# Performance work log

Hardware: AMD Instinct MI355X
Metric: run time of the kernel (lower is better)

Reference implementation:

```python
import jax, jax.numpy as jnp
import numpy as np

NUM_CLASSES = 1000
B, Q, N = 64, 900, 30
NO_OBJ_W = 0.1
COST_CLASS, COST_BBOX, COST_GIOU = 1.0, 5.0, 2.0
LOSS_BBOX, LOSS_GIOU = 5.0, 2.0


def cxcywh_to_xyxy(b):
    cx, cy, w, h = b[..., 0], b[..., 1], b[..., 2], b[..., 3]
    return jnp.stack([cx - 0.5 * w, cy - 0.5 * h, cx + 0.5 * w, cy + 0.5 * h], axis=-1)


def _area(b):
    return jnp.clip(b[..., 2] - b[..., 0], 0.0) * jnp.clip(b[..., 3] - b[..., 1], 0.0)


def giou_xyxy(b1, b2):
    # GIoU over broadcastable [..., 4] xyxy boxes
    lt = jnp.maximum(b1[..., :2], b2[..., :2])
    rb = jnp.minimum(b1[..., 2:], b2[..., 2:])
    wh = jnp.clip(rb - lt, 0.0)
    inter = wh[..., 0] * wh[..., 1]
    union = _area(b1) + _area(b2) - inter
    iou = inter / jnp.maximum(union, 1e-6)
    ltc = jnp.minimum(b1[..., :2], b2[..., :2])
    rbc = jnp.maximum(b1[..., 2:], b2[..., 2:])
    whc = jnp.clip(rbc - ltc, 0.0)
    ac = whc[..., 0] * whc[..., 1]
    return iou - (ac - union) / jnp.maximum(ac, 1e-6)


def _cost_matrices(pred_logits, pred_boxes, tgt_labels, tgt_boxes_xyxy):
    prob = jax.nn.softmax(pred_logits, axis=-1)                    # [B,Q,C+1]
    cost_cls = -jax.vmap(lambda p, l: p[:, l])(prob, tgt_labels)   # [B,Q,N]
    pred_xyxy = jnp.clip(cxcywh_to_xyxy(pred_boxes), 0.0, 1.0)     # [B,Q,4]
    cost_l1 = jnp.sum(jnp.abs(pred_xyxy[:, :, None] - tgt_boxes_xyxy[:, None]), -1)
    cost_g = -giou_xyxy(pred_xyxy[:, :, None], tgt_boxes_xyxy[:, None])
    C = COST_CLASS * cost_cls + COST_BBOX * cost_l1 + COST_GIOU * cost_g
    return C, pred_xyxy


def greedy_match(C):
    # faithful to the module's torch fallback matcher: iteratively pick the
    # global minimum of the cost matrix, masking used rows/cols (host-side,
    # non-differentiable, exactly like the detach->cpu->assignment in torch)
    Cw = C.copy()
    Qn, Nn = Cw.shape
    rows, cols = [], []
    for _ in range(min(Qn, Nn)):
        i = int(np.argmin(Cw))
        pi, ti = divmod(i, Nn)
        rows.append(pi)
        cols.append(ti)
        Cw[pi, :] = 1e9
        Cw[:, ti] = 1e9
    return np.array(rows, dtype=np.int32), np.array(cols, dtype=np.int32)


def match_all(Cnp):
    pis, tis = zip(*[greedy_match(Cnp[b]) for b in range(Cnp.shape[0])])
    return jnp.asarray(np.stack(pis)), jnp.asarray(np.stack(tis))  # [B,N] each


def set_losses(pred_logits, pred_xyxy, tgt_labels, tgt_boxes_xyxy, pi, ti):
    ce_weight = jnp.ones(NUM_CLASSES + 1, jnp.float32).at[NUM_CLASSES].set(NO_OBJ_W)
    bidx = jnp.arange(B)[:, None]
    # target class per query: matched -> tgt label, else no-object class
    tc = jnp.full((B, Q), NUM_CLASSES, dtype=jnp.int32)
    tc = tc.at[bidx, pi].set(jnp.take_along_axis(tgt_labels, ti, axis=1))
    nll = -jnp.take_along_axis(jax.nn.log_softmax(pred_logits, -1), tc[..., None].astype(jnp.int32), axis=2)[..., 0]
    w = ce_weight[tc]
    ce = jnp.mean(jnp.sum(w * nll, axis=1) / jnp.sum(w, axis=1))  # torch weighted CE mean, per image
    p_m = pred_xyxy[bidx, pi]          # [B,N,4] matched preds
    t_m = tgt_boxes_xyxy[bidx, ti]     # [B,N,4] matched targets
    l1 = jnp.mean(jnp.mean(jnp.abs(p_m - t_m), axis=(1, 2)))
    gl = jnp.mean(jnp.mean(1.0 - giou_xyxy(p_m, t_m), axis=1))
    total = ce + LOSS_BBOX * l1 + LOSS_GIOU * gl
    return jnp.stack([total, ce, l1, gl])


def setup_inputs():
    key = jax.random.key(0)
    k1, k2, k3, k4, k5 = jax.random.split(key, 5)
    pred_logits = jax.random.normal(k1, (B, Q, NUM_CLASSES + 1), jnp.float32)
    pred_boxes = jax.random.uniform(k2, (B, Q, 4), jnp.float32, 0.05, 0.95)
    tgt_labels = jax.random.randint(k3, (B, N), 0, NUM_CLASSES, dtype=jnp.int32)
    lt = jax.random.uniform(k4, (B, N, 2), jnp.float32, 0.0, 0.6)
    wh = jax.random.uniform(k5, (B, N, 2), jnp.float32, 0.02, 0.37)
    tgt_boxes_xyxy = jnp.concatenate([lt, lt + wh], axis=-1)  # valid 0..1 xyxy
    return {"pred_logits": pred_logits, "pred_boxes": pred_boxes,
            "tgt_labels": tgt_labels, "tgt_boxes_xyxy": tgt_boxes_xyxy}


def reference(pred_logits, pred_boxes, tgt_labels, tgt_boxes_xyxy):
    C, pred_xyxy = _cost_matrices(pred_logits, pred_boxes, tgt_labels, tgt_boxes_xyxy)
    pi, ti = match_all(np.asarray(jax.lax.stop_gradient(C)))
    # returns [loss_total, loss_ce, loss_bbox, loss_giou]
    return set_losses(pred_logits, pred_xyxy, tgt_labels, tgt_boxes_xyxy, pi, ti)
```

## Files before the change

kernel.cpp:

```cpp
#include <hip/hip_runtime.h>
#include <math.h>

#define BB 64
#define QQ 900
#define NN 30
#define C1 1001
#define QN (QQ * NN)
#define NO_OBJ_W 0.1f

__device__ __align__(16) unsigned g_ordT[BB * NN * QQ];
__device__ unsigned long long g_top[BB * NN * NN];
__device__ float  g_logZ[BB * QQ];
__device__ float  g_noobj[BB * QQ];
__device__ float4 g_xyxy[BB * QQ];
__device__ float  g_acc[3];
__device__ unsigned g_cnt;

__device__ __forceinline__ float giou_f(float ax1, float ay1, float ax2, float ay2,
                                        float bx1, float by1, float bx2, float by2) {
    float ix1 = fmaxf(ax1, bx1), iy1 = fmaxf(ay1, by1);
    float ix2 = fminf(ax2, bx2), iy2 = fminf(ay2, by2);
    float iw = fmaxf(ix2 - ix1, 0.f), ih = fmaxf(iy2 - iy1, 0.f);
    float inter = iw * ih;
    float areaA = fmaxf(ax2 - ax1, 0.f) * fmaxf(ay2 - ay1, 0.f);
    float areaB = fmaxf(bx2 - bx1, 0.f) * fmaxf(by2 - by1, 0.f);
    float uni = areaA + areaB - inter;
    float iou = inter / fmaxf(uni, 1e-6f);
    float cx1 = fminf(ax1, bx1), cy1 = fminf(ay1, by1);
    float cx2 = fmaxf(ax2, bx2), cy2 = fmaxf(ay2, by2);
    float cw = fmaxf(cx2 - cx1, 0.f), ch = fmaxf(cy2 - cy1, 0.f);
    float ac = cw * ch;
    return iou - (ac - uni) / fmaxf(ac, 1e-6f);
}

__device__ __forceinline__ unsigned ord_map(float f) {
    unsigned u = __float_as_uint(f);
    return (u & 0x80000000u) ? ~u : (u | 0x80000000u);
}

__global__ __launch_bounds__(256) void cost_kernel(const float* __restrict__ logits,
                                                   const float* __restrict__ pboxes,
                                                   const int*   __restrict__ labels,
                                                   const float* __restrict__ tboxes) {
    if (blockIdx.x == 0 && threadIdx.x == 0) {
        g_acc[0] = 0.f; g_acc[1] = 0.f; g_acc[2] = 0.f;
        g_cnt = 0u;
    }
    int tid = threadIdx.x;
    int lane = tid & 63, wid = tid >> 6;
    int gwave = blockIdx.x * 4 + wid;
    int b = gwave / QQ;

    __shared__ unsigned s_c[4][NN];

    size_t s = (size_t)gwave * C1;
    size_t a0 = (s + 3) >> 2;
    size_t a1 = (s + C1) >> 2;
    int nq = (int)(a1 - a0);
    int hh = (int)(a0 * 4 - s);
    int tt = (int)((s + C1) - a1 * 4);

    int lab = 0;
    float rl = 0.f;
    if (lane < NN) {
        lab = labels[b * NN + lane];
        rl = logits[s + lab];
    }
    float row1000 = logits[s + 1000];
    float4 tbv = make_float4(0.f, 0.f, 0.f, 0.f);
    if (lane < NN) tbv = *(const float4*)(tboxes + ((size_t)(b * NN + lane)) * 4);

    const float4* L4 = (const float4*)logits;
    float4 v4[4];
#pragma unroll
    for (int i = 0; i < 4; ++i) {
        int qq = lane + 64 * i;
        v4[i] = (qq < nq) ? L4[a0 + qq]
                          : make_float4(-INFINITY, -INFINITY, -INFINITY, -INFINITY);
    }
    float e1 = (lane < hh) ? logits[s + lane] : -INFINITY;
    float e2 = (lane < tt) ? logits[a1 * 4 + lane] : -INFINITY;

    float sm = __expf(e1) + __expf(e2);
#pragma unroll
    for (int i = 0; i < 4; ++i) {
        sm += __expf(v4[i].x);
        sm += __expf(v4[i].y);
        sm += __expf(v4[i].z);
        sm += __expf(v4[i].w);
    }
#pragma unroll
    for (int off = 32; off; off >>= 1) sm += __shfl_xor(sm, off);
    float logZ = __logf(sm);

    const float* pb = pboxes + (size_t)gwave * 4;
    float cx = pb[0], cy = pb[1], w = pb[2], h = pb[3];
    float x1 = fminf(fmaxf(cx - 0.5f * w, 0.f), 1.f);
    float y1 = fminf(fmaxf(cy - 0.5f * h, 0.f), 1.f);
    float x2 = fminf(fmaxf(cx + 0.5f * w, 0.f), 1.f);
    float y2 = fminf(fmaxf(cy + 0.5f * h, 0.f), 1.f);

    if (lane == 0) {
        g_logZ[gwave] = logZ;
        g_noobj[gwave] = logZ - row1000;
        g_xyxy[gwave] = make_float4(x1, y1, x2, y2);
    }

    if (lane < NN) {
        int t = lane;
        float pcls = __expf(rl - logZ);
        float tx1 = tbv.x, ty1 = tbv.y, tx2 = tbv.z, ty2 = tbv.w;
        float l1 = fabsf(x1 - tx1) + fabsf(y1 - ty1) + fabsf(x2 - tx2) + fabsf(y2 - ty2);
        float g = giou_f(x1, y1, x2, y2, tx1, ty1, tx2, ty2);
        s_c[wid][t] = ord_map(-pcls + 5.0f * l1 - 2.0f * g);
    }
    __syncthreads();

    if (tid < NN) {
        int t = tid;
        int q0 = (blockIdx.x % 225) * 4;
        int b0 = blockIdx.x / 225;
        uint4 v = make_uint4(s_c[0][t], s_c[1][t], s_c[2][t], s_c[3][t]);
        *(uint4*)&g_ordT[((size_t)(b0 * NN + t)) * QQ + q0] = v;
    }
}

__global__ __launch_bounds__(256) void select_kernel() {
    int gw = (blockIdx.x * blockDim.x + threadIdx.x) >> 6;
    int lane = threadIdx.x & 63;
    if (gw >= BB * NN) return;
    int t = gw % NN;

    const unsigned* col = g_ordT + (size_t)gw * QQ;
    unsigned long long key[16];
#pragma unroll
    for (int j = 0; j < 15; ++j) {
        int q = j * 64 + lane;
        if (q < QQ) {
            unsigned o = col[q];
            key[j] = ((unsigned long long)o << 32) | (unsigned)(q * NN + t);
        } else {
            key[j] = ~0ull;
        }
    }
    key[15] = ~0ull;

#pragma unroll
    for (int kk = 2; kk <= 16; kk <<= 1) {
#pragma unroll
        for (int jj = kk >> 1; jj > 0; jj >>= 1) {
#pragma unroll
            for (int i = 0; i < 16; ++i) {
                int l = i ^ jj;
                if (l > i) {
                    bool up = ((i & kk) == 0);
                    unsigned long long a = key[i], c = key[l];
                    bool sw = up ? (a > c) : (a < c);
                    key[i] = sw ? c : a;
                    key[l] = sw ? a : c;
                }
            }
        }
    }

    unsigned long long* outp = g_top + (size_t)gw * NN;
#pragma unroll 1
    for (int r = 0; r < NN / 2; ++r) {
        unsigned long long m1 = key[0];
        unsigned long long m2 = key[1];
#pragma unroll
        for (int off = 32; off; off >>= 1) {
            unsigned long long o1 = __shfl_xor(m1, off);
            unsigned long long o2 = __shfl_xor(m2, off);
            unsigned long long lo = (o1 < m1) ? o1 : m1;
            unsigned long long hi = (o1 < m1) ? m1 : o1;
            unsigned long long n2 = (o2 < m2) ? o2 : m2;
            m1 = lo;
            m2 = (hi < n2) ? hi : n2;
        }
        if (lane == 2 * r)     outp[2 * r]     = m1;
        if (lane == 2 * r + 1) outp[2 * r + 1] = m2;
        if (key[0] == m1 || key[0] == m2) {
#pragma unroll
            for (int j = 0; j < 15; ++j) key[j] = key[j + 1];
            key[15] = ~0ull;
        }
        if (key[0] == m2) {
#pragma unroll
            for (int j = 0; j < 15; ++j) key[j] = key[j + 1];
            key[15] = ~0ull;
        }
    }
}

__global__ __launch_bounds__(256) void match_loss_kernel(const float* __restrict__ logits,
                                                         const int*   __restrict__ labels,
                                                         const float* __restrict__ tboxes,
                                                         float* __restrict__ out) {
    int b = blockIdx.x;
    int tid = threadIdx.x;

    __shared__ unsigned long long s_cand[NN * NN];
    __shared__ int s_pi[NN], s_ti[NN];
    __shared__ unsigned s_dead[29];
    __shared__ float s4[4][4];

    const unsigned long long* topb = g_top + (size_t)b * NN * NN;
    for (int i = tid; i < NN * NN; i += 256) s_cand[i] = topb[i];
    if (tid < 29) s_dead[tid] = 0u;
    __syncthreads();

    if (tid < 64) {
        int lane = tid;
        bool colLive = lane < NN;
        int ptr = 0;
        unsigned long long cand = colLive ? s_cand[lane * NN] : ~0ull;
        unsigned rowc = colLive ? ((unsigned)cand) / NN : 0u;

        int it = 0;
        while (it < NN) {
            unsigned long long m1 = colLive ? cand : ~0ull;
            unsigned long long m2 = ~0ull;
#pragma unroll
            for (int off = 32; off; off >>= 1) {
                unsigned long long o1 = __shfl_xor(m1, off);
                unsigned long long o2 = __shfl_xor(m2, off);
                unsigned long long lo = (o1 < m1) ? o1 : m1;
                unsigned long long hi = (o1 < m1) ? m1 : o1;
                unsigned long long n2 = (o2 < m2) ? o2 : m2;
                m1 = lo;
                m2 = (hi < n2) ? hi : n2;
            }
            unsigned e1 = (unsigned)m1;
            int q1 = e1 / NN, t1 = e1 - (e1 / NN) * NN;
            unsigned e2 = (unsigned)m2;
            int q2 = e2 / NN, t2 = e2 - (e2 / NN) * NN;
            bool acc2 = (m2 != ~0ull) && (it + 1 < NN) && (q2 != q1) && (t2 != t1);

            if (lane == 0) {
                s_pi[it] = q1;
                s_ti[it] = t1;
                s_dead[q1 >> 5] |= (1u << (q1 & 31));
                if (acc2) {
                    s_pi[it + 1] = q2;
                    s_ti[it + 1] = t2;
                    s_dead[q2 >> 5] |= (1u << (q2 & 31));
                }
            }
            if (lane == t1) colLive = false;
            if (acc2 && lane == t2) colLive = false;
            if (colLive && (rowc == (unsigned)q1 || (acc2 && rowc == (unsigned)q2))) {
                do {
                    ++ptr;
                    cand = s_cand[lane * NN + ptr];
                    rowc = ((unsigned)cand) / NN;
                } while ((s_dead[rowc >> 5] >> (rowc & 31)) & 1u);
            }
            it += acc2 ? 2 : 1;
        }
    }
    __syncthreads();

    float sA = 0.f;
    for (int q = tid; q < QQ; q += 256) sA += g_noobj[b * QQ + q];

    float sB = 0.f, sL = 0.f, sG = 0.f;
    if (tid < NN) {
        int pq = s_pi[tid], pt = s_ti[tid];
        int gq = b * QQ + pq;
        int lab = labels[b * NN + pt];
        float mnll = g_logZ[gq] - logits[(size_t)gq * C1 + lab];
        sB = mnll - NO_OBJ_W * g_noobj[gq];
        float4 p = g_xyxy[gq];
        const float* tb = tboxes + ((size_t)(b * NN + pt)) * 4;
        float tx1 = tb[0], ty1 = tb[1], tx2 = tb[2], ty2 = tb[3];
        sL = fabsf(p.x - tx1) + fabsf(p.y - ty1) + fabsf(p.z - tx2) + fabsf(p.w - ty2);
        sG = 1.0f - giou_f(p.x, p.y, p.z, p.w, tx1, ty1, tx2, ty2);
    }

    int lane = tid & 63, wid = tid >> 6;
    float vv[4] = {sA, sB, sL, sG};
#pragma unroll
    for (int j = 0; j < 4; ++j) {
        float x = vv[j];
#pragma unroll
        for (int off = 32; off; off >>= 1) x += __shfl_xor(x, off);
        if (lane == 0) s4[wid][j] = x;
    }
    __syncthreads();
    if (tid == 0) {
        float a = 0.f, bs = 0.f, l = 0.f, g = 0.f;
        for (int w = 0; w < 4; ++w) { a += s4[w][0]; bs += s4[w][1]; l += s4[w][2]; g += s4[w][3]; }
        atomicAdd(&g_acc[0], NO_OBJ_W * a + bs);
        atomicAdd(&g_acc[1], l);
        atomicAdd(&g_acc[2], g);
        __threadfence();
        unsigned prev = atomicAdd(&g_cnt, 1u);
        if (prev == BB - 1) {
            __threadfence();
            float ce = atomicAdd(&g_acc[0], 0.f) / (float)(BB * 117);
            float l1 = atomicAdd(&g_acc[1], 0.f) / (float)(BB * NN * 4);
            float gl = atomicAdd(&g_acc[2], 0.f) / (float)(BB * NN);
            out[0] = ce + 5.0f * l1 + 2.0f * gl;
            out[1] = ce;
            out[2] = l1;
            out[3] = gl;
        }
    }
}

extern "C" void kernel_launch(void* const* d_in, const int* in_sizes, int n_in,
                              void* d_out, int out_size, void* d_ws, size_t ws_size,
                              hipStream_t stream) {
    const float* pred_logits = (const float*)d_in[0];
    const float* pred_boxes  = (const float*)d_in[1];
    const int*   tgt_labels  = (const int*)d_in[2];
    const float* tgt_boxes   = (const float*)d_in[3];
    float* out = (float*)d_out;

    cost_kernel<<<(BB * QQ) / 4, 256, 0, stream>>>(pred_logits, pred_boxes, tgt_labels, tgt_boxes);
    select_kernel<<<(BB * NN) / 4, 256, 0, stream>>>();
    match_loss_kernel<<<BB, 256, 0, stream>>>(pred_logits, tgt_labels, tgt_boxes, out);
}
```

Before: 84.80 us.

## Split per-column top-k selection across two waves and merge halves

The select kernel now gives each cost column to two waves, each sorting and extracting the top 30 from half of the 900 queries. The two sorted halves are then merged by rank using binary search in shared memory. This halves the register sort depth and per-wave serial extraction at the cost of twice as many waves plus a merge step. The no-object sum in the match kernel is also moved onto the idle waves so it runs alongside the serial greedy matching.

```diff
diff --git a/kernel.cpp b/kernel.cpp
--- a/kernel.cpp
+++ b/kernel.cpp
@@ -7,6 +7,7 @@
 #define C1 1001
 #define QN (QQ * NN)
 #define NO_OBJ_W 0.1f
+#define HQ 450
 
 __device__ __align__(16) unsigned g_ordT[BB * NN * QQ];
 __device__ unsigned long long g_top[BB * NN * NN];
@@ -60,10 +61,9 @@
     int hh = (int)(a0 * 4 - s);
     int tt = (int)((s + C1) - a1 * 4);
 
-    int lab = 0;
     float rl = 0.f;
     if (lane < NN) {
-        lab = labels[b * NN + lane];
+        int lab = labels[b * NN + lane];
         rl = logits[s + lab];
     }
     float row1000 = logits[s + 1000];
@@ -107,12 +107,10 @@
     }
 
     if (lane < NN) {
-        int t = lane;
         float pcls = __expf(rl - logZ);
-        float tx1 = tbv.x, ty1 = tbv.y, tx2 = tbv.z, ty2 = tbv.w;
-        float l1 = fabsf(x1 - tx1) + fabsf(y1 - ty1) + fabsf(x2 - tx2) + fabsf(y2 - ty2);
-        float g = giou_f(x1, y1, x2, y2, tx1, ty1, tx2, ty2);
-        s_c[wid][t] = ord_map(-pcls + 5.0f * l1 - 2.0f * g);
+        float l1 = fabsf(x1 - tbv.x) + fabsf(y1 - tbv.y) + fabsf(x2 - tbv.z) + fabsf(y2 - tbv.w);
+        float g = giou_f(x1, y1, x2, y2, tbv.x, tbv.y, tbv.z, tbv.w);
+        s_c[wid][lane] = ord_map(-pcls + 5.0f * l1 - 2.0f * g);
     }
     __syncthreads();
 
@@ -126,31 +124,37 @@
 }
 
 __global__ __launch_bounds__(256) void select_kernel() {
-    int gw = (blockIdx.x * blockDim.x + threadIdx.x) >> 6;
-    int lane = threadIdx.x & 63;
-    if (gw >= BB * NN) return;
+    int tid = threadIdx.x;
+    int lane = tid & 63, wid = tid >> 6;
+    int gw = blockIdx.x * 2 + (wid >> 1);
+    int h = wid & 1;
     int t = gw % NN;
 
-    const unsigned* col = g_ordT + (size_t)gw * QQ;
-    unsigned long long key[16];
-#pragma unroll
-    for (int j = 0; j < 15; ++j) {
-        int q = j * 64 + lane;
-        if (q < QQ) {
-            unsigned o = col[q];
-            key[j] = ((unsigned long long)o << 32) | (unsigned)(q * NN + t);
-        } else {
-            key[j] = ~0ull;
-        }
-    }
-    key[15] = ~0ull;
-
-#pragma unroll
-    for (int kk = 2; kk <= 16; kk <<= 1) {
+    __shared__ unsigned long long s_half[4][NN];
+
+    const unsigned* col = g_ordT + (size_t)gw * QQ + h * HQ;
+    int qbase = h * HQ;
+
+    unsigned long long key[8];
+#pragma unroll
+    for (int j = 0; j < 7; ++j) {
+        int ql = j * 64 + lane;
+        unsigned o = col[ql];
+        key[j] = ((unsigned long long)o << 32) | (unsigned)((qbase + ql) * NN + t);
+    }
+    {
+        int ql = 448 + lane;
+        key[7] = (lane < 2)
+            ? (((unsigned long long)col[ql] << 32) | (unsigned)((qbase + ql) * NN + t))
+            : ~0ull;
+    }
+
+#pragma unroll
+    for (int kk = 2; kk <= 8; kk <<= 1) {
 #pragma unroll
         for (int jj = kk >> 1; jj > 0; jj >>= 1) {
 #pragma unroll
-            for (int i = 0; i < 16; ++i) {
+            for (int i = 0; i < 8; ++i) {
                 int l = i ^ jj;
                 if (l > i) {
                     bool up = ((i & kk) == 0);
@@ -163,7 +167,6 @@
         }
     }
 
-    unsigned long long* outp = g_top + (size_t)gw * NN;
 #pragma unroll 1
     for (int r = 0; r < NN / 2; ++r) {
         unsigned long long m1 = key[0];
@@ -178,17 +181,38 @@
             m1 = lo;
             m2 = (hi < n2) ? hi : n2;
         }
-        if (lane == 2 * r)     outp[2 * r]     = m1;
-        if (lane == 2 * r + 1) outp[2 * r + 1] = m2;
+        if (lane == 2 * r)     s_half[wid][2 * r]     = m1;
+        if (lane == 2 * r + 1) s_half[wid][2 * r + 1] = m2;
         if (key[0] == m1 || key[0] == m2) {
 #pragma unroll
-            for (int j = 0; j < 15; ++j) key[j] = key[j + 1];
-            key[15] = ~0ull;
+            for (int j = 0; j < 7; ++j) key[j] = key[j + 1];
+            key[7] = ~0ull;
         }
         if (key[0] == m2) {
 #pragma unroll
-            for (int j = 0; j < 15; ++j) key[j] = key[j + 1];
-            key[15] = ~0ull;
+            for (int j = 0; j < 7; ++j) key[j] = key[j + 1];
+            key[7] = ~0ull;
+        }
+    }
+    __syncthreads();
+
+    if ((wid & 1) == 0) {
+        const unsigned long long* A = s_half[wid];
+        const unsigned long long* B = s_half[wid + 1];
+        unsigned long long mykey = ~0ull;
+        const unsigned long long* other = B;
+        int myidx = -1;
+        if (lane < NN)                  { mykey = A[lane];      other = B; myidx = lane; }
+        else if (lane >= 32 && lane < 32 + NN) { mykey = B[lane - 32]; other = A; myidx = lane - 32; }
+        if (myidx >= 0) {
+            int lo = 0, hi = NN;
+            while (lo < hi) {
+                int mid = (lo + hi) >> 1;
+                if (other[mid] < mykey) lo = mid + 1;
+                else hi = mid;
+            }
+            int pos = myidx + lo;
+            if (pos < NN) g_top[(size_t)gw * NN + pos] = mykey;
         }
     }
 }
@@ -210,7 +234,10 @@
     if (tid < 29) s_dead[tid] = 0u;
     __syncthreads();
 
-    if (tid < 64) {
+    float sA = 0.f;
+    if (tid >= 64) {
+        for (int q = tid - 64; q < QQ; q += 192) sA += g_noobj[b * QQ + q];
+    } else {
         int lane = tid;
         bool colLive = lane < NN;
         int ptr = 0;
@@ -260,9 +287,6 @@
         }
     }
     __syncthreads();
-
-    float sA = 0.f;
-    for (int q = tid; q < QQ; q += 256) sA += g_noobj[b * QQ + q];
 
     float sB = 0.f, sL = 0.f, sG = 0.f;
     if (tid < NN) {
@@ -319,6 +343,6 @@
     float* out = (float*)d_out;
 
     cost_kernel<<<(BB * QQ) / 4, 256, 0, stream>>>(pred_logits, pred_boxes, tgt_labels, tgt_boxes);
-    select_kernel<<<(BB * NN) / 4, 256, 0, stream>>>();
+    select_kernel<<<(BB * NN) / 2, 256, 0, stream>>>();
     match_loss_kernel<<<BB, 256, 0, stream>>>(pred_logits, tgt_labels, tgt_boxes, out);
 }
```

Result: slower. 92.75 us (+9.4%).

## Replace per-column bitonic top-k with histogram threshold selection plus small sort

Applied to the files above, without the earlier changes.

The select kernel now finds the 30 smallest costs per target column differently. It builds a 256-bin shared-memory histogram over the column's value range, finds the bin holding the 30th element with a prefix scan, compacts the candidates at or below that bin with ballot, and bitonic-sorts up to 64 of them across the wave. If more than 64 candidates fall at or below the threshold, it falls back to the old register sort and 15-round extraction. This avoids the per-lane 16-element sort and the serial shuffle-reduction extraction loop, at the cost of atomics, two block barriers and a data-dependent fallback branch.

```diff
diff --git a/kernel.cpp b/kernel.cpp
--- a/kernel.cpp
+++ b/kernel.cpp
@@ -60,10 +60,9 @@
     int hh = (int)(a0 * 4 - s);
     int tt = (int)((s + C1) - a1 * 4);
 
-    int lab = 0;
     float rl = 0.f;
     if (lane < NN) {
-        lab = labels[b * NN + lane];
+        int lab = labels[b * NN + lane];
         rl = logits[s + lab];
     }
     float row1000 = logits[s + 1000];
@@ -107,12 +106,10 @@
     }
 
     if (lane < NN) {
-        int t = lane;
         float pcls = __expf(rl - logZ);
-        float tx1 = tbv.x, ty1 = tbv.y, tx2 = tbv.z, ty2 = tbv.w;
-        float l1 = fabsf(x1 - tx1) + fabsf(y1 - ty1) + fabsf(x2 - tx2) + fabsf(y2 - ty2);
-        float g = giou_f(x1, y1, x2, y2, tx1, ty1, tx2, ty2);
-        s_c[wid][t] = ord_map(-pcls + 5.0f * l1 - 2.0f * g);
+        float l1 = fabsf(x1 - tbv.x) + fabsf(y1 - tbv.y) + fabsf(x2 - tbv.z) + fabsf(y2 - tbv.w);
+        float g = giou_f(x1, y1, x2, y2, tbv.x, tbv.y, tbv.z, tbv.w);
+        s_c[wid][lane] = ord_map(-pcls + 5.0f * l1 - 2.0f * g);
     }
     __syncthreads();
 
@@ -126,69 +123,169 @@
 }
 
 __global__ __launch_bounds__(256) void select_kernel() {
-    int gw = (blockIdx.x * blockDim.x + threadIdx.x) >> 6;
-    int lane = threadIdx.x & 63;
+    int tid = threadIdx.x;
+    int lane = tid & 63, wid = tid >> 6;
+    int gw = (blockIdx.x * 256 + tid) >> 6;
     if (gw >= BB * NN) return;
     int t = gw % NN;
 
+    __shared__ unsigned s_hist[4][256];
+    __shared__ unsigned long long s_cand[4][64];
+
     const unsigned* col = g_ordT + (size_t)gw * QQ;
+    bool act = lane < 60;
     unsigned long long key[16];
+    unsigned ordv[15];
 #pragma unroll
     for (int j = 0; j < 15; ++j) {
-        int q = j * 64 + lane;
-        if (q < QQ) {
+        if (act) {
+            int q = j * 60 + lane;
             unsigned o = col[q];
+            ordv[j] = o;
             key[j] = ((unsigned long long)o << 32) | (unsigned)(q * NN + t);
         } else {
+            ordv[j] = 0u;
             key[j] = ~0ull;
         }
     }
     key[15] = ~0ull;
 
-#pragma unroll
-    for (int kk = 2; kk <= 16; kk <<= 1) {
-#pragma unroll
-        for (int jj = kk >> 1; jj > 0; jj >>= 1) {
-#pragma unroll
-            for (int i = 0; i < 16; ++i) {
-                int l = i ^ jj;
-                if (l > i) {
-                    bool up = ((i & kk) == 0);
-                    unsigned long long a = key[i], c = key[l];
-                    bool sw = up ? (a > c) : (a < c);
-                    key[i] = sw ? c : a;
-                    key[l] = sw ? a : c;
+    unsigned mn = act ? ordv[0] : 0xFFFFFFFFu;
+    unsigned mx = act ? ordv[0] : 0u;
+#pragma unroll
+    for (int j = 1; j < 15; ++j) {
+        if (act) {
+            mn = (ordv[j] < mn) ? ordv[j] : mn;
+            mx = (ordv[j] > mx) ? ordv[j] : mx;
+        }
+    }
+#pragma unroll
+    for (int off = 32; off; off >>= 1) {
+        unsigned on = (unsigned)__shfl_xor((int)mn, off);
+        unsigned ox = (unsigned)__shfl_xor((int)mx, off);
+        mn = (on < mn) ? on : mn;
+        mx = (ox > mx) ? ox : mx;
+    }
+    float inv = 256.0f / ((float)(mx - mn) + 1.0f);
+
+#pragma unroll
+    for (int i = 0; i < 4; ++i) s_hist[wid][i * 64 + lane] = 0u;
+    __syncthreads();
+#pragma unroll
+    for (int j = 0; j < 15; ++j) {
+        if (act) {
+            int bin = (int)((float)(ordv[j] - mn) * inv);
+            bin = (bin > 255) ? 255 : bin;
+            atomicAdd(&s_hist[wid][bin], 1u);
+        }
+    }
+    __syncthreads();
+
+    unsigned cs[4];
+    cs[0] = s_hist[wid][4 * lane + 0];
+    cs[1] = s_hist[wid][4 * lane + 1];
+    cs[2] = s_hist[wid][4 * lane + 2];
+    cs[3] = s_hist[wid][4 * lane + 3];
+    unsigned lsum = cs[0] + cs[1] + cs[2] + cs[3];
+    unsigned incl = lsum;
+    for (int off = 1; off < 64; off <<= 1) {
+        unsigned v = (unsigned)__shfl_up((int)incl, off);
+        if (lane >= off) incl += v;
+    }
+    unsigned run = incl - lsum;
+    int Tl = 0;
+    unsigned Ncl = 0;
+#pragma unroll
+    for (int i = 0; i < 4; ++i) {
+        unsigned ce = run + cs[i];
+        if (run < (unsigned)NN && ce >= (unsigned)NN) { Tl = 4 * lane + i; Ncl = ce; }
+        run = ce;
+    }
+#pragma unroll
+    for (int off = 32; off; off >>= 1) {
+        Tl  += __shfl_xor(Tl, off);
+        Ncl += (unsigned)__shfl_xor((int)Ncl, off);
+    }
+
+    unsigned long long* outp = g_top + (size_t)gw * NN;
+
+    if (Ncl <= 64u) {
+        unsigned base = 0;
+#pragma unroll
+        for (int j = 0; j < 15; ++j) {
+            bool take = false;
+            if (act) {
+                int bin = (int)((float)(ordv[j] - mn) * inv);
+                bin = (bin > 255) ? 255 : bin;
+                take = (bin <= Tl);
+            }
+            unsigned long long mask = __ballot(take);
+            if (take) {
+                int pos = (int)base + __popcll(mask & ((1ull << lane) - 1ull));
+                s_cand[wid][pos] = key[j];
+            }
+            base += (unsigned)__popcll(mask);
+        }
+        asm volatile("s_waitcnt lgkmcnt(0)" ::: "memory");
+        unsigned long long ck = (lane < (int)base) ? s_cand[wid][lane] : ~0ull;
+#pragma unroll
+        for (int k = 2; k <= 64; k <<= 1) {
+#pragma unroll
+            for (int j2 = k >> 1; j2 > 0; j2 >>= 1) {
+                unsigned long long pr = __shfl_xor(ck, j2);
+                bool up = ((lane & k) == 0);
+                bool lower = ((lane & j2) == 0);
+                bool keepmin = (lower == up);
+                unsigned long long mnk = (ck < pr) ? ck : pr;
+                unsigned long long mxk = (ck < pr) ? pr : ck;
+                ck = keepmin ? mnk : mxk;
+            }
+        }
+        if (lane < NN) outp[lane] = ck;
+    } else {
+#pragma unroll
+        for (int kk = 2; kk <= 16; kk <<= 1) {
+#pragma unroll
+            for (int jj = kk >> 1; jj > 0; jj >>= 1) {
+#pragma unroll
+                for (int i = 0; i < 16; ++i) {
+                    int l = i ^ jj;
+                    if (l > i) {
+                        bool up = ((i & kk) == 0);
+                        unsigned long long a = key[i], c = key[l];
+                        bool sw = up ? (a > c) : (a < c);
+                        key[i] = sw ? c : a;
+                        key[l] = sw ? a : c;
+                    }
                 }
             }
         }
-    }
-
-    unsigned long long* outp = g_top + (size_t)gw * NN;
 #pragma unroll 1
-    for (int r = 0; r < NN / 2; ++r) {
-        unsigned long long m1 = key[0];
-        unsigned long long m2 = key[1];
-#pragma unroll
-        for (int off = 32; off; off >>= 1) {
-            unsigned long long o1 = __shfl_xor(m1, off);
-            unsigned long long o2 = __shfl_xor(m2, off);
-            unsigned long long lo = (o1 < m1) ? o1 : m1;
-            unsigned long long hi = (o1 < m1) ? m1 : o1;
-            unsigned long long n2 = (o2 < m2) ? o2 : m2;
-            m1 = lo;
-            m2 = (hi < n2) ? hi : n2;
-        }
-        if (lane == 2 * r)     outp[2 * r]     = m1;
-        if (lane == 2 * r + 1) outp[2 * r + 1] = m2;
-        if (key[0] == m1 || key[0] == m2) {
-#pragma unroll
-            for (int j = 0; j < 15; ++j) key[j] = key[j + 1];
-            key[15] = ~0ull;
-        }
-        if (key[0] == m2) {
-#pragma unroll
-            for (int j = 0; j < 15; ++j) key[j] = key[j + 1];
-            key[15] = ~0ull;
+        for (int r = 0; r < NN / 2; ++r) {
+            unsigned long long m1 = key[0];
+            unsigned long long m2 = key[1];
+#pragma unroll
+            for (int off = 32; off; off >>= 1) {
+                unsigned long long o1 = __shfl_xor(m1, off);
+                unsigned long long o2 = __shfl_xor(m2, off);
+                unsigned long long lo = (o1 < m1) ? o1 : m1;
+                unsigned long long hi = (o1 < m1) ? m1 : o1;
+                unsigned long long n2 = (o2 < m2) ? o2 : m2;
+                m1 = lo;
+                m2 = (hi < n2) ? hi : n2;
+            }
+            if (lane == 2 * r)     outp[2 * r]     = m1;
+            if (lane == 2 * r + 1) outp[2 * r + 1] = m2;
+            if (key[0] == m1 || key[0] == m2) {
+#pragma unroll
+                for (int j = 0; j < 15; ++j) key[j] = key[j + 1];
+                key[15] = ~0ull;
+            }
+            if (key[0] == m2) {
+#pragma unroll
+                for (int j = 0; j < 15; ++j) key[j] = key[j + 1];
+                key[15] = ~0ull;
+            }
         }
     }
 }
```

After: 89.22 us. 1.05x slower.
